# Kernel tuning notes

Measured on AMD Instinct MI355X. Metric: run time of the kernel, lower is better.

The kernel has to match this reference:

```python
import jax, jax.numpy as jnp
import numpy as np

N = 4000; T_GRU = 32; T_TREE = 16; F = 256; HS = 128; H = 3 * HS; CC = 512; E = 64000; D4 = 4 * HS


def _gru_last(x, wi, wh, bi, bh):
    # x: [N, T, F]; torch GRU gate order r, z, n. Returns last hidden [N, H].
    xp = jnp.einsum('ntf,gf->ntg', x, wi) + bi  # [N, T, 3H]
    h0 = jnp.zeros((x.shape[0], wh.shape[1]), x.dtype)
    def step(h, xt):
        gh = h @ wh.T + bh
        ir, iz, inn = jnp.split(xt, 3, axis=1)
        hr, hz, hn = jnp.split(gh, 3, axis=1)
        r = jax.nn.sigmoid(ir + hr)
        z = jax.nn.sigmoid(iz + hz)
        n = jnp.tanh(inn + r * hn)
        return (1.0 - z) * n + z * h, None
    hT, _ = jax.lax.scan(step, h0, jnp.swapaxes(xp, 0, 1))
    return hT


def _tree_root(x, ioux_w, ioux_b, iouh_w, iouh_b, fx_w, fx_b, fh_w, fh_b):
    # Chain-structured TreeLSTM (each node has one child); x: [N, T, F], leaf-to-root.
    xi = jnp.einsum('ntf,gf->ntg', x, ioux_w) + ioux_b  # [N, T, 3M]
    xf = jnp.einsum('ntf,mf->ntm', x, fx_w) + fx_b      # [N, T, M]
    M = fh_w.shape[0]
    z0 = jnp.zeros((x.shape[0], M), x.dtype)
    def step(carry, xs):
        c, h = carry
        xi_t, xf_t = xs
        iou = xi_t + h @ iouh_w.T + iouh_b
        i, o, u = jnp.split(iou, 3, axis=1)
        f = jax.nn.sigmoid(xf_t + h @ fh_w.T + fh_b)
        c = jax.nn.sigmoid(i) * jnp.tanh(u) + f * c
        h = jax.nn.sigmoid(o) * jnp.tanh(c)
        return (c, h), None
    (c, h), _ = jax.lax.scan(step, (z0, z0), (jnp.swapaxes(xi, 0, 1), jnp.swapaxes(xf, 0, 1)))
    return h


def _gcn(x, w, b, row, col):
    # PyG GCNConv: self-loops + symmetric normalization.
    n = x.shape[0]
    xw = x @ w.T
    loops = jnp.arange(n, dtype=row.dtype)
    r = jnp.concatenate([row, loops])
    c = jnp.concatenate([col, loops])
    deg = jax.ops.segment_sum(jnp.ones(r.shape, x.dtype), c, num_segments=n)
    dinv = jnp.where(deg > 0, jax.lax.rsqrt(jnp.maximum(deg, 1e-12)), 0.0)
    norm = (dinv[r] * dinv[c])[:, None]
    return jax.ops.segment_sum(xw[r] * norm, c, num_segments=n) + b


def setup_inputs() -> dict:
    key = jax.random.key(0)
    ks = jax.random.split(key, 48)
    s = 0.05
    p = lambda i, sh: jax.random.normal(ks[i], sh, jnp.float32) * s
    return {
        'feat1': p(0, (N, T_GRU, F)),
        'feat2': p(1, (N, T_TREE, F)),
        'feat3': p(2, (N, T_TREE, F)),
        'feat4': p(3, (N, CC)),
        'edge_index': jax.random.randint(ks[4], (2, E), 0, N),
        'gru_wi': p(5, (3 * H, F)), 'gru_wh': p(6, (3 * H, H)),
        'gru_bi': p(7, (3 * H,)), 'gru_bh': p(8, (3 * H,)),
        't1_ioux_w': p(9, (3 * H, F)), 't1_ioux_b': p(10, (3 * H,)),
        't1_iouh_w': p(11, (3 * H, H)), 't1_iouh_b': p(12, (3 * H,)),
        't1_fx_w': p(13, (H, F)), 't1_fx_b': p(14, (H,)),
        't1_fh_w': p(15, (H, H)), 't1_fh_b': p(16, (H,)),
        't2_ioux_w': p(17, (3 * H, F)), 't2_ioux_b': p(18, (3 * H,)),
        't2_iouh_w': p(19, (3 * H, H)), 't2_iouh_b': p(20, (3 * H,)),
        't2_fx_w': p(21, (H, F)), 't2_fx_b': p(22, (H,)),
        't2_fh_w': p(23, (H, H)), 't2_fh_b': p(24, (H,)),
        'r1_w': p(25, (HS, H)), 'r1_b': p(26, (HS,)),
        'r2_w': p(27, (HS, H)), 'r2_b': p(28, (HS,)),
        'r3_w': p(29, (HS, H)), 'r3_b': p(30, (HS,)),
        'r4_w': p(31, (HS, CC)), 'r4_b': p(32, (HS,)),
        'gcn0_w': p(33, (D4, D4)), 'gcn0_b': p(34, (D4,)),
        'gcn1_w': p(35, (D4, D4)), 'gcn1_b': p(36, (D4,)),
        'r7_w': p(37, (2, D4)), 'r7_b': p(38, (2,)),
    }


def reference(feat1, feat2, feat3, feat4, edge_index,
              gru_wi, gru_wh, gru_bi, gru_bh,
              t1_ioux_w, t1_ioux_b, t1_iouh_w, t1_iouh_b, t1_fx_w, t1_fx_b, t1_fh_w, t1_fh_b,
              t2_ioux_w, t2_ioux_b, t2_iouh_w, t2_iouh_b, t2_fx_w, t2_fx_b, t2_fh_w, t2_fh_b,
              r1_w, r1_b, r2_w, r2_b, r3_w, r3_b, r4_w, r4_b,
              gcn0_w, gcn0_b, gcn1_w, gcn1_b, r7_w, r7_b):
    v1 = _gru_last(feat1, gru_wi, gru_wh, gru_bi, gru_bh)            # [N, H]
    v2 = _tree_root(feat2, t1_ioux_w, t1_ioux_b, t1_iouh_w, t1_iouh_b, t1_fx_w, t1_fx_b, t1_fh_w, t1_fh_b)
    v3 = _tree_root(feat3, t2_ioux_w, t2_ioux_b, t2_iouh_w, t2_iouh_b, t2_fx_w, t2_fx_b, t2_fh_w, t2_fh_b)
    f1 = v1 @ r1_w.T + r1_b
    f2 = v2 @ r2_w.T + r2_b
    f3 = v3 @ r3_w.T + r3_b
    f4 = feat4 @ r4_w.T + r4_b
    m = jnp.concatenate([f1, f2, f3, f4], axis=1)                    # [N, 4*HS]
    row, col = edge_index[0], edge_index[1]
    m = jax.nn.relu(_gcn(m, gcn0_w, gcn0_b, row, col))
    m = _gcn(m, gcn1_w, gcn1_b, row, col)
    m = jax.nn.softmax(m @ r7_w.T + r7_b, axis=1)                    # [N, 2]
    return m.T                                                       # [2, N]
```

## Files before the change

### kernel.cpp

```cpp
#include <hip/hip_runtime.h>
#include <hip/hip_bf16.h>
#include <math.h>

#define NN 4000
#define TG 32
#define TT 16
#define FF 256
#define HH 384
#define GCOLS 1536
#define KCAT 640
#define EE 64000
#define D4 512

typedef __attribute__((ext_vector_type(8))) short short8;
typedef __attribute__((ext_vector_type(8))) unsigned short ushort8v;
typedef __attribute__((ext_vector_type(4))) float float4v;

static __device__ __forceinline__ float fsig(float x)  { return 1.0f / (1.0f + __expf(-x)); }
static __device__ __forceinline__ float ftanh(float x) { return 2.0f / (1.0f + __expf(-2.0f*x)) - 1.0f; }
static __device__ __forceinline__ unsigned short f2bf(float f) {
    __hip_bfloat16 h = __float2bfloat16(f); return *reinterpret_cast<unsigned short*>(&h);
}
static __device__ __forceinline__ float bf2f(unsigned short u) {
    union { unsigned int i; float f; } x; x.i = ((unsigned int)u) << 16; return x.f;
}

static __device__ __forceinline__ void async_copy16(const void* g, void* l) {
    __builtin_amdgcn_global_load_lds(
        (const __attribute__((address_space(1))) unsigned int*)g,
        (__attribute__((address_space(3))) unsigned int*)l, 16, 0, 0);
}

static __device__ __forceinline__ void xcd_swz(int& bx, int& by, int& bz) {
    const int gx = gridDim.x, gy = gridDim.y;
    const int nwg = gx * gy * gridDim.z;
    const int w = (blockIdx.z * gy + blockIdx.y) * gx + blockIdx.x;
    const int q = nwg >> 3, r = nwg & 7;
    const int xcd = w & 7, i = w >> 3;
    const int L = (xcd < r ? xcd*(q+1) : r*(q+1) + (xcd - r)*q) + i;
    bx = L % gx; int rest = L / gx;
    by = rest % gy; bz = rest / gy;
}

__global__ __launch_bounds__(256) void prep_w_kernel(
    const float* __restrict__ gwi, const float* __restrict__ gwh,
    const float* __restrict__ gbi, const float* __restrict__ gbh,
    const float* __restrict__ x1w, const float* __restrict__ x1b,
    const float* __restrict__ h1w, const float* __restrict__ h1b,
    const float* __restrict__ fx1w, const float* __restrict__ fx1b,
    const float* __restrict__ fh1w, const float* __restrict__ fh1b,
    const float* __restrict__ x2w, const float* __restrict__ x2b,
    const float* __restrict__ h2w, const float* __restrict__ h2b,
    const float* __restrict__ fx2w, const float* __restrict__ fx2b,
    const float* __restrict__ fh2w, const float* __restrict__ fh2b,
    __hip_bfloat16* __restrict__ Wx, __hip_bfloat16* __restrict__ Wh,
    float* __restrict__ bp)
{
    int z = blockIdx.z;
    int idx = blockIdx.x * 256 + threadIdx.x;
    int c = idx / KCAT, k = idx - c * KCAT;
    int bx = c >> 7, wc = (c >> 6) & 1, g = (c >> 4) & 3, rl = c & 15;
    int j = bx*32 + wc*16 + rl;
    float v = 0.0f, bv = 0.0f;
    if (z == 0) {
        if (g <= 1) {
            int row = g*HH + j;
            v = (k < FF) ? gwi[row*FF + k] : gwh[row*HH + (k-FF)];
            bv = gbi[row] + gbh[row];
        } else if (g == 2) {
            int row = 2*HH + j;
            v = (k < FF) ? gwi[row*FF + k] : 0.0f;
            bv = gbi[row];
        } else {
            int row = 2*HH + j;
            v = (k < FF) ? 0.0f : gwh[row*HH + (k-FF)];
            bv = gbh[row];
        }
    } else {
        const float* xw  = (z==1)? x1w  : x2w;   const float* xb  = (z==1)? x1b  : x2b;
        const float* hw  = (z==1)? h1w  : h2w;   const float* hb_ = (z==1)? h1b  : h2b;
        const float* fxw = (z==1)? fx1w : fx2w;  const float* fxb = (z==1)? fx1b : fx2b;
        const float* fhw = (z==1)? fh1w : fh2w;  const float* fhb = (z==1)? fh1b : fh2b;
        if (g < 3) {
            int row = g*HH + j;
            v = (k < FF) ? xw[row*FF + k] : hw[row*HH + (k-FF)];
            bv = xb[row] + hb_[row];
        } else {
            v = (k < FF) ? fxw[j*FF + k] : fhw[j*HH + (k-FF)];
            bv = fxb[j] + fhb[j];
        }
    }
    if (k < FF) Wx[(size_t)z*GCOLS*FF + (size_t)c*FF + k] = __float2bfloat16(v);
    else        Wh[(size_t)z*GCOLS*HH + (size_t)c*HH + (k-FF)] = __float2bfloat16(v);
    if (k == 0) bp[z*GCOLS + c] = bv;
}

#define C0 (TG*NN*FF/8)
#define C1 (C0 + TT*NN*FF/8)
#define C2 (C1 + TT*NN*FF/8)
#define C3 (C2 + NN*D4/8)
#define C4 (C3 + 128*HH/8)
#define C5 (C4 + 128*HH/8)
#define C6 (C5 + 128*HH/8)
#define C7 (C6 + 128*D4/8)
#define C8 (C7 + D4*D4/8)
#define C9 (C8 + D4*D4/8)

__global__ __launch_bounds__(256) void conv_all_kernel(
    const float* __restrict__ f1, const float* __restrict__ f2, const float* __restrict__ f3,
    const float* __restrict__ f4, const float* __restrict__ r1w, const float* __restrict__ r2w,
    const float* __restrict__ r3w, const float* __restrict__ r4w,
    const float* __restrict__ g0w, const float* __restrict__ g1w,
    __hip_bfloat16* __restrict__ xg, __hip_bfloat16* __restrict__ xt,
    __hip_bfloat16* __restrict__ f4b, __hip_bfloat16* __restrict__ rw123,
    __hip_bfloat16* __restrict__ r4w16, __hip_bfloat16* __restrict__ g0w16,
    __hip_bfloat16* __restrict__ g1w16)
{
    int i = blockIdx.x*256 + threadIdx.x;
    if (i >= C9) return;
    const float* s; __hip_bfloat16* d; int off;
    if      (i < C0) { s = f1;  d = xg;                      off = i; }
    else if (i < C1) { s = f2;  d = xt;                      off = i - C0; }
    else if (i < C2) { s = f3;  d = xt + (size_t)TT*NN*FF;   off = i - C1; }
    else if (i < C3) { s = f4;  d = f4b;                     off = i - C2; }
    else if (i < C4) { s = r1w; d = rw123;                   off = i - C3; }
    else if (i < C5) { s = r2w; d = rw123 + 128*HH;          off = i - C4; }
    else if (i < C6) { s = r3w; d = rw123 + 2*128*HH;        off = i - C5; }
    else if (i < C7) { s = r4w; d = r4w16;                   off = i - C6; }
    else if (i < C8) { s = g0w; d = g0w16;                   off = i - C7; }
    else             { s = g1w; d = g1w16;                   off = i - C8; }
    float4 v0 = ((const float4*)s)[off*2];
    float4 v1 = ((const float4*)s)[off*2 + 1];
    ushort8v u;
    u[0] = f2bf(v0.x); u[1] = f2bf(v0.y); u[2] = f2bf(v0.z); u[3] = f2bf(v0.w);
    u[4] = f2bf(v1.x); u[5] = f2bf(v1.y); u[6] = f2bf(v1.z); u[7] = f2bf(v1.w);
    ((ushort8v*)d)[off] = u;
}

#define BM 128
#define BN 128
#define BKK 32

__global__ __launch_bounds__(256) void gemm0_k(
    const __hip_bfloat16* __restrict__ Ab, size_t zA, int lda,
    const __hip_bfloat16* __restrict__ Wb, size_t zW, int K,
    const float* __restrict__ bias, size_t zB,
    float* __restrict__ C, size_t zC,
    __hip_bfloat16* __restrict__ C16, size_t zC16,
    int ldC, int M)
{
    const int z = blockIdx.z;
    const __hip_bfloat16* A = Ab + zA*z;
    const __hip_bfloat16* W = Wb + zW*z;

    __shared__ __align__(16) __hip_bfloat16 As[BM][BKK];
    __shared__ __align__(16) __hip_bfloat16 Bs[BN][BKK];

    const int tid  = threadIdx.x;
    const int lane = tid & 63;
    const int w    = tid >> 6;
    const int wr = w >> 1, wc = w & 1;
    const int rowBase = blockIdx.y * BM;
    const int colBase = blockIdx.x * BN;
    const int sRow = tid >> 2;
    const int sK   = (tid & 3) * 8;

    float4v acc[4][4];
    #pragma unroll
    for (int i = 0; i < 4; ++i)
        #pragma unroll
        for (int j = 0; j < 4; ++j)
            acc[i][j] = (float4v){0.f, 0.f, 0.f, 0.f};

    const int rl = lane & 15;
    const int kl = (lane >> 4) * 8;

    for (int kt = 0; kt < K; kt += BKK) {
        const int kk = kt + sK;
        #pragma unroll
        for (int i = 0; i < 2; ++i) {
            int gr = rowBase + i*64 + sRow;
            if (gr > M-1) gr = M-1;
            async_copy16(A + (size_t)gr*lda + kk, &As[i*64 + sRow][sK]);
        }
        #pragma unroll
        for (int i = 0; i < 2; ++i) {
            int r = i*64 + sRow;
            async_copy16(W + (size_t)(colBase + r)*K + kk, &Bs[r][sK]);
        }
        __syncthreads();

        short8 af[4], bfr[4];
        #pragma unroll
        for (int mi = 0; mi < 4; ++mi)
            af[mi] = *(const short8*)&As[wr*64 + mi*16 + rl][kl];
        #pragma unroll
        for (int ni = 0; ni < 4; ++ni)
            bfr[ni] = *(const short8*)&Bs[wc*64 + ni*16 + rl][kl];
        #pragma unroll
        for (int mi = 0; mi < 4; ++mi)
            #pragma unroll
            for (int ni = 0; ni < 4; ++ni)
                acc[mi][ni] = __builtin_amdgcn_mfma_f32_16x16x32_bf16(af[mi], bfr[ni], acc[mi][ni], 0, 0, 0);
        __syncthreads();
    }

    const int rq = (lane >> 4) * 4;
    float* Cz = C ? (C + zC*z) : nullptr;
    __hip_bfloat16* C16z = C16 ? (C16 + zC16*z) : nullptr;
    #pragma unroll
    for (int mi = 0; mi < 4; ++mi) {
        #pragma unroll
        for (int q = 0; q < 4; ++q) {
            int row = rowBase + wr*64 + mi*16 + rq + q;
            if (row >= M) continue;
            #pragma unroll
            for (int ni = 0; ni < 4; ++ni) {
                int col = colBase + wc*64 + ni*16 + rl;
                float v = acc[mi][ni][q];
                if (bias) v += bias[zB*z + col];
                if (Cz)   Cz[(size_t)row*ldC + col] = v;
                if (C16z) C16z[(size_t)row*ldC + col] = __float2bfloat16(v);
            }
        }
    }
}

struct StepSet {
    const __hip_bfloat16 *X, *Hin, *Wx, *Wh;
    const float *bp;
    const __hip_bfloat16 *Sin;
    __hip_bfloat16 *Sout, *Hout;
    int lda, xoff;
};

#define NT (KCAT/BKK)
#define SBM 64

template<int MODE>
__global__ __launch_bounds__(256) void step_k(StepSet S)
{
    int bxi, byi, bzi;
    xcd_swz(bxi, byi, bzi);

    const __hip_bfloat16* X  = S.X;
    const __hip_bfloat16* Hi = S.Hin;
    const __hip_bfloat16* Wx = S.Wx;
    const __hip_bfloat16* Wh = S.Wh;
    const float* bp = S.bp;
    const __hip_bfloat16* Si = S.Sin;
    __hip_bfloat16* So = S.Sout;
    __hip_bfloat16* Ho = S.Hout;
    const int lda = S.lda, xoff = S.xoff;

    __shared__ __align__(16) __hip_bfloat16 As[3][SBM][BKK];
    __shared__ __align__(16) __hip_bfloat16 Bs[3][BN][BKK];

    const int tid  = threadIdx.x;
    const int lane = tid & 63;
    const int w    = tid >> 6;
    const int wr = w >> 1, wc = w & 1;
    const int rowBase = byi * SBM;
    const int colBase = bxi * BN;

    const int sR  = tid >> 2;
    const int sC  = tid & 3;
    const int sSw = sC ^ ((sR >> 1) & 3);
    int gra = rowBase + sR; if (gra > NN-1) gra = NN-1;

    auto stage = [&](int buf, int kt) {
        if (kt < FF) {
            const int kk = kt + sSw*8;
            async_copy16(X  + (size_t)gra*lda + xoff + kk,          &As[buf][sR][sC*8]);
            async_copy16(Wx + (size_t)(colBase + sR)*FF + kk,       &Bs[buf][sR][sC*8]);
            async_copy16(Wx + (size_t)(colBase + 64 + sR)*FF + kk,  &Bs[buf][64 + sR][sC*8]);
        } else {
            const int kk = kt - FF + sSw*8;
            async_copy16(Hi + (size_t)gra*HH + kk,                  &As[buf][sR][sC*8]);
            async_copy16(Wh + (size_t)(colBase + sR)*HH + kk,       &Bs[buf][sR][sC*8]);
            async_copy16(Wh + (size_t)(colBase + 64 + sR)*HH + kk,  &Bs[buf][64 + sR][sC*8]);
        }
    };

    float4v acc[2][4];
    #pragma unroll
    for (int i = 0; i < 2; ++i)
        #pragma unroll
        for (int j = 0; j < 4; ++j)
            acc[i][j] = (float4v){0.f, 0.f, 0.f, 0.f};

    const int rl = lane & 15;
    const int dF = (lane >> 4) ^ ((rl >> 1) & 3);

    stage(0, 0);
    stage(1, BKK);

    #pragma unroll
    for (int it = 0; it < NT; ++it) {
        if (it < NT-1) asm volatile("s_waitcnt vmcnt(3)" ::: "memory");
        else           asm volatile("s_waitcnt vmcnt(0)" ::: "memory");
        __builtin_amdgcn_sched_barrier(0);
        __builtin_amdgcn_s_barrier();
        __builtin_amdgcn_sched_barrier(0);
        if (it + 2 < NT) stage((it+2)%3, (it+2)*BKK);
        __builtin_amdgcn_sched_barrier(0);

        const int cur = it % 3;
        short8 af[2], bfr[4];
        #pragma unroll
        for (int mi = 0; mi < 2; ++mi)
            af[mi] = *(const short8*)&As[cur][wr*32 + mi*16 + rl][dF*8];

        const bool xph = (it*BKK) < FF;
        if (MODE == 2) {
            #pragma unroll
            for (int ni = 0; ni < 4; ++ni)
                bfr[ni] = *(const short8*)&Bs[cur][wc*64 + ni*16 + rl][dF*8];
            asm volatile("s_waitcnt lgkmcnt(0)" ::: "memory");
            __builtin_amdgcn_sched_barrier(0);
            #pragma unroll
            for (int mi = 0; mi < 2; ++mi)
                #pragma unroll
                for (int ni = 0; ni < 4; ++ni)
                    acc[mi][ni] = __builtin_amdgcn_mfma_f32_16x16x32_bf16(af[mi], bfr[ni], acc[mi][ni], 0, 0, 0);
        } else if (xph) {
            #pragma unroll
            for (int ni = 0; ni < 3; ++ni)
                bfr[ni] = *(const short8*)&Bs[cur][wc*64 + ni*16 + rl][dF*8];
            asm volatile("s_waitcnt lgkmcnt(0)" ::: "memory");
            __builtin_amdgcn_sched_barrier(0);
            #pragma unroll
            for (int mi = 0; mi < 2; ++mi)
                #pragma unroll
                for (int ni = 0; ni < 3; ++ni)
                    acc[mi][ni] = __builtin_amdgcn_mfma_f32_16x16x32_bf16(af[mi], bfr[ni], acc[mi][ni], 0, 0, 0);
        } else {
            bfr[0] = *(const short8*)&Bs[cur][wc*64 + 0*16 + rl][dF*8];
            bfr[1] = *(const short8*)&Bs[cur][wc*64 + 1*16 + rl][dF*8];
            bfr[3] = *(const short8*)&Bs[cur][wc*64 + 3*16 + rl][dF*8];
            asm volatile("s_waitcnt lgkmcnt(0)" ::: "memory");
            __builtin_amdgcn_sched_barrier(0);
            #pragma unroll
            for (int mi = 0; mi < 2; ++mi) {
                acc[mi][0] = __builtin_amdgcn_mfma_f32_16x16x32_bf16(af[mi], bfr[0], acc[mi][0], 0, 0, 0);
                acc[mi][1] = __builtin_amdgcn_mfma_f32_16x16x32_bf16(af[mi], bfr[1], acc[mi][1], 0, 0, 0);
                acc[mi][3] = __builtin_amdgcn_mfma_f32_16x16x32_bf16(af[mi], bfr[3], acc[mi][3], 0, 0, 0);
            }
        }
    }

    const int rq = (lane >> 4) * 4;
    const int j  = (colBase >> 2) + wc*16 + rl;
    const int cb = colBase + wc*64 + rl;
    float b0 = bp[cb + 0];
    float b1 = bp[cb + 16];
    float b2 = bp[cb + 32];
    float b3 = bp[cb + 48];

    #pragma unroll
    for (int mi = 0; mi < 2; ++mi) {
        #pragma unroll
        for (int q = 0; q < 4; ++q) {
            int row = rowBase + wr*32 + mi*16 + rq + q;
            if (row >= NN) continue;
            float g0 = acc[mi][0][q] + b0;
            float g1 = acc[mi][1][q] + b1;
            float g2 = acc[mi][2][q] + b2;
            float g3 = acc[mi][3][q] + b3;
            size_t off = (size_t)row*HH + j;
            if (MODE == 1) {
                float r  = fsig(g0), zz = fsig(g1);
                float n  = ftanh(g2 + r*g3);
                float hp = __bfloat162float(Hi[off]);
                float hn = (1.0f - zz)*n + zz*hp;
                Ho[off] = __float2bfloat16(hn);
            } else {
                float cp = __bfloat162float(Si[off]);
                float cn = fsig(g0)*ftanh(g2) + fsig(g3)*cp;
                So[off] = __float2bfloat16(cn);
                float hn = fsig(g1)*ftanh(cn);
                Ho[off] = __float2bfloat16(hn);
            }
        }
    }
}

__global__ __launch_bounds__(256) void count_kernel(const int* __restrict__ col, int* __restrict__ degi)
{
    int e = blockIdx.x*256 + threadIdx.x;
    if (e < EE) atomicAdd(&degi[col[e]], 1);
}

__global__ __launch_bounds__(1024) void scan_kernel(const int* __restrict__ degi,
    int* __restrict__ start, int* __restrict__ cursor, float* __restrict__ dinv)
{
    __shared__ int s[1024];
    int t = threadIdx.x;
    int v[4]; int sum = 0;
    #pragma unroll
    for (int i = 0; i < 4; ++i) {
        int idx = t*4 + i;
        v[i] = (idx < NN) ? degi[idx] : 0;
        sum += v[i];
    }
    s[t] = sum;
    __syncthreads();
    for (int d = 1; d < 1024; d <<= 1) {
        int x = (t >= d) ? s[t-d] : 0;
        __syncthreads();
        s[t] += x;
        __syncthreads();
    }
    int base = s[t] - sum;
    int run = 0;
    #pragma unroll
    for (int i = 0; i < 4; ++i) {
        int idx = t*4 + i;
        if (idx < NN) {
            int st = base + run;
            start[idx] = st;
            cursor[idx] = st;
            dinv[idx] = rsqrtf((float)v[i] + 1.0f);
        }
        run += v[i];
    }
    if (t == 1023) start[NN] = s[1023];
}

__global__ __launch_bounds__(256) void fill_kernel(const int* __restrict__ row,
    const int* __restrict__ col, int* __restrict__ cursor, int* __restrict__ esrc)
{
    int e = blockIdx.x*256 + threadIdx.x;
    if (e < EE) {
        int c = col[e];
        int pos = atomicAdd(&cursor[c], 1);
        esrc[pos] = row[e];
    }
}

__global__ __launch_bounds__(256) void gather_kernel(const __hip_bfloat16* __restrict__ xw,
    const int* __restrict__ esrc, const int* __restrict__ start,
    const float* __restrict__ dinv, const float* __restrict__ bias,
    float* __restrict__ mout, __hip_bfloat16* __restrict__ mout16, int relu)
{
    int wv = threadIdx.x >> 6, lane = threadIdx.x & 63;
    int n = blockIdx.x*4 + wv;
    if (n >= NN) return;
    float a[8] = {0.f,0.f,0.f,0.f,0.f,0.f,0.f,0.f};
    int s0 = start[n], s1 = start[n+1];
    float dn = dinv[n];
    for (int e = s0; e < s1; ++e) {
        int r = esrc[e];
        float nrm = dinv[r]*dn;
        ushort8v v = *(const ushort8v*)(xw + (size_t)r*D4 + lane*8);
        #pragma unroll
        for (int i = 0; i < 8; ++i) a[i] += bf2f(v[i])*nrm;
    }
    ushort8v u = *(const ushort8v*)(xw + (size_t)n*D4 + lane*8);
    float dd = dn*dn;
    #pragma unroll
    for (int i = 0; i < 8; ++i) {
        float vv = a[i] + bf2f(u[i])*dd + bias[lane*8 + i];
        if (relu) vv = fmaxf(vv, 0.0f);
        if (mout)   mout[(size_t)n*D4 + lane*8 + i] = vv;
        if (mout16) mout16[(size_t)n*D4 + lane*8 + i] = __float2bfloat16(vv);
    }
}

__global__ __launch_bounds__(256) void final_kernel(const float* __restrict__ m,
    const float* __restrict__ w, const float* __restrict__ b, float* __restrict__ out)
{
    int wave = threadIdx.x >> 6;
    int lane = threadIdx.x & 63;
    int n = blockIdx.x*4 + wave;
    const float* row = m + (size_t)n*D4 + lane*8;
    float4 v0 = *(const float4*)(row);
    float4 v1 = *(const float4*)(row + 4);
    const float* w0 = w + lane*8;
    const float* w1 = w + D4 + lane*8;
    float4 u0 = *(const float4*)(w0); float4 u1 = *(const float4*)(w0 + 4);
    float4 t0 = *(const float4*)(w1); float4 t1 = *(const float4*)(w1 + 4);
    float a = v0.x*u0.x + v0.y*u0.y + v0.z*u0.z + v0.w*u0.w
            + v1.x*u1.x + v1.y*u1.y + v1.z*u1.z + v1.w*u1.w;
    float bb = v0.x*t0.x + v0.y*t0.y + v0.z*t0.z + v0.w*t0.w
             + v1.x*t1.x + v1.y*t1.y + v1.z*t1.z + v1.w*t1.w;
    #pragma unroll
    for (int s = 32; s; s >>= 1) { a += __shfl_xor(a, s); bb += __shfl_xor(bb, s); }
    if (lane == 0) {
        float l0 = a + b[0], l1 = bb + b[1];
        float mx = fmaxf(l0, l1);
        float e0 = expf(l0 - mx), e1 = expf(l1 - mx);
        float s = e0 + e1;
        out[n]      = e0 / s;
        out[NN + n] = e1 / s;
    }
}

extern "C" void kernel_launch(void* const* d_in, const int* in_sizes, int n_in,
                              void* d_out, int out_size, void* d_ws, size_t ws_size,
                              hipStream_t stream)
{
    const float* feat1 = (const float*)d_in[0];
    const float* feat2 = (const float*)d_in[1];
    const float* feat3 = (const float*)d_in[2];
    const float* feat4 = (const float*)d_in[3];
    const int*   eidx  = (const int*)d_in[4];
    const float* r1w = (const float*)d_in[25]; const float* r1b = (const float*)d_in[26];
    const float* r2w = (const float*)d_in[27]; const float* r2b = (const float*)d_in[28];
    const float* r3w = (const float*)d_in[29]; const float* r3b = (const float*)d_in[30];
    const float* r4w = (const float*)d_in[31]; const float* r4b = (const float*)d_in[32];
    const float* g0w = (const float*)d_in[33]; const float* g0b = (const float*)d_in[34];
    const float* g1w = (const float*)d_in[35]; const float* g1b = (const float*)d_in[36];
    const float* r7w = (const float*)d_in[37]; const float* r7b = (const float*)d_in[38];

    float* ws = (float*)d_ws;
    size_t o = 0;
    auto alloc = [&](size_t nfl) { float* p = ws + o; o += (nfl + 3) & ~(size_t)3; return p; };

    __hip_bfloat16* hb0 = (__hip_bfloat16*)alloc((size_t)3*NN*HH/2);
    __hip_bfloat16* cb0 = (__hip_bfloat16*)alloc((size_t)NN*HH);
    size_t zeroFloats = o;
    __hip_bfloat16* hb1 = (__hip_bfloat16*)alloc((size_t)3*NN*HH/2);
    __hip_bfloat16* cb1 = (__hip_bfloat16*)alloc((size_t)NN*HH);
    __hip_bfloat16* xg  = (__hip_bfloat16*)alloc((size_t)TG*NN*FF/2);
    __hip_bfloat16* xt  = (__hip_bfloat16*)alloc((size_t)2*TT*NN*FF/2);
    __hip_bfloat16* Wx  = (__hip_bfloat16*)alloc((size_t)3*GCOLS*FF/2);
    __hip_bfloat16* Wh  = (__hip_bfloat16*)alloc((size_t)3*GCOLS*HH/2);
    float* bp   = alloc(3*GCOLS);
    float* mbuf = alloc((size_t)NN*D4);
    __hip_bfloat16* xwb16 = (__hip_bfloat16*)alloc((size_t)NN*D4/2);
    float* dinv = alloc(NN);
    __hip_bfloat16* mbf16 = (__hip_bfloat16*)alloc((size_t)NN*D4/2);
    __hip_bfloat16* f4b   = (__hip_bfloat16*)alloc((size_t)NN*D4/2);
    __hip_bfloat16* rw123 = (__hip_bfloat16*)alloc((size_t)3*128*HH/2);
    float* rb123 = alloc(3*128);
    __hip_bfloat16* r4w16 = (__hip_bfloat16*)alloc((size_t)128*D4/2);
    __hip_bfloat16* g0w16 = (__hip_bfloat16*)alloc((size_t)D4*D4/2);
    __hip_bfloat16* g1w16 = (__hip_bfloat16*)alloc((size_t)D4*D4/2);
    int* degi   = (int*)alloc(NN);
    int* start  = (int*)alloc(NN + 4);
    int* cursor = (int*)alloc(NN);
    int* esrc   = (int*)alloc(EE);

    __hip_bfloat16* hbp[2] = {hb0, hb1};
    __hip_bfloat16* cbp[2] = {cb0, cb1};

    hipMemsetAsync(hb0, 0, zeroFloats*sizeof(float), stream);
    hipMemsetAsync(degi, 0, NN*sizeof(int), stream);

    prep_w_kernel<<<dim3(3840,1,3),256,0,stream>>>(
        (const float*)d_in[5],(const float*)d_in[6],(const float*)d_in[7],(const float*)d_in[8],
        (const float*)d_in[9],(const float*)d_in[10],(const float*)d_in[11],(const float*)d_in[12],
        (const float*)d_in[13],(const float*)d_in[14],(const float*)d_in[15],(const float*)d_in[16],
        (const float*)d_in[17],(const float*)d_in[18],(const float*)d_in[19],(const float*)d_in[20],
        (const float*)d_in[21],(const float*)d_in[22],(const float*)d_in[23],(const float*)d_in[24],
        Wx, Wh, bp);

    conv_all_kernel<<<(C9 + 255)/256,256,0,stream>>>(
        feat1, feat2, feat3, feat4, r1w, r2w, r3w, r4w, g0w, g1w,
        xg, xt, f4b, rw123, r4w16, g0w16, g1w16);
    hipMemcpyAsync(rb123,       r1b, 128*sizeof(float), hipMemcpyDeviceToDevice, stream);
    hipMemcpyAsync(rb123 + 128, r2b, 128*sizeof(float), hipMemcpyDeviceToDevice, stream);
    hipMemcpyAsync(rb123 + 256, r3b, 128*sizeof(float), hipMemcpyDeviceToDevice, stream);

    count_kernel<<<250,256,0,stream>>>(eidx + EE, degi);
    scan_kernel<<<1,1024,0,stream>>>(degi, start, cursor, dinv);
    fill_kernel<<<250,256,0,stream>>>(eidx, eidx + EE, cursor, esrc);

    for (int t = 0; t < TG; ++t) {
        int p = t & 1, q = p ^ 1;
        StepSet Gs = { xg, hbp[p], Wx, Wh, bp,
                       hbp[p], hbp[q], hbp[q], TG*FF, t*FF };
        step_k<1><<<dim3(GCOLS/BN, 63, 1),256,0,stream>>>(Gs);
    }
    for (int tr = 0; tr < 2; ++tr) {
        for (int t = 0; t < TT; ++t) {
            int p = t & 1, q = p ^ 1;
            StepSet Ts = { xt + (size_t)tr*TT*NN*FF,
                           hbp[p] + (size_t)(1+tr)*NN*HH,
                           Wx + (size_t)(1+tr)*GCOLS*FF,
                           Wh + (size_t)(1+tr)*GCOLS*HH,
                           bp + (size_t)(1+tr)*GCOLS,
                           cbp[p] + (size_t)tr*NN*HH,
                           cbp[q] + (size_t)tr*NN*HH,
                           hbp[q] + (size_t)(1+tr)*NN*HH,
                           TT*FF, t*FF };
            step_k<2><<<dim3(GCOLS/BN, 63, 1),256,0,stream>>>(Ts);
        }
    }

    gemm0_k<<<dim3(1,32,3),256,0,stream>>>(
        hbp[0], (size_t)NN*HH, HH, rw123, (size_t)128*HH, HH, rb123, 128,
        nullptr, 0, mbf16, 128, D4, NN);
    gemm0_k<<<dim3(1,32,1),256,0,stream>>>(
        f4b, 0, D4, r4w16, 0, D4, r4b, 0,
        nullptr, 0, mbf16 + 384, 0, D4, NN);

    gemm0_k<<<dim3(4,32,1),256,0,stream>>>(
        mbf16, 0, D4, g0w16, 0, D4, nullptr, 0,
        nullptr, 0, xwb16, 0, D4, NN);
    gather_kernel<<<1000,256,0,stream>>>(xwb16, esrc, start, dinv, g0b, nullptr, mbf16, 1);

    gemm0_k<<<dim3(4,32,1),256,0,stream>>>(
        mbf16, 0, D4, g1w16, 0, D4, nullptr, 0,
        nullptr, 0, xwb16, 0, D4, NN);
    gather_kernel<<<1000,256,0,stream>>>(xwb16, esrc, start, dinv, g1b, mbuf, nullptr, 0);

    final_kernel<<<1000,256,0,stream>>>(mbuf, r7w, r7b, (float*)d_out);
}
```

Before: 1.459 ms.

## Fuse fp32-to-bf16 input conversion into recurrent step kernels and merge prep launches

Step kernels now read the fp32 feature sequences directly, hold them in registers and convert to bf16 into shared memory, instead of a separate pass converting all of feat1/2/3 into bf16 buffers. The remaining small conversions, the bias copies and the degree count are merged into one prep kernel, which removes several launches and memcpys. This avoids a large read-and-write pass over the features, but each step kernel now reads twice as many bytes for its X tiles and carries extra registers plus changed wait-count bookkeeping.

```diff
diff --git a/kernel.cpp b/kernel.cpp
--- a/kernel.cpp
+++ b/kernel.cpp
@@ -95,46 +95,49 @@
     if (k == 0) bp[z*GCOLS + c] = bv;
 }
 
-#define C0 (TG*NN*FF/8)
-#define C1 (C0 + TT*NN*FF/8)
-#define C2 (C1 + TT*NN*FF/8)
-#define C3 (C2 + NN*D4/8)
-#define C4 (C3 + 128*HH/8)
-#define C5 (C4 + 128*HH/8)
-#define C6 (C5 + 128*HH/8)
-#define C7 (C6 + 128*D4/8)
-#define C8 (C7 + D4*D4/8)
-#define C9 (C8 + D4*D4/8)
-
-__global__ __launch_bounds__(256) void conv_all_kernel(
-    const float* __restrict__ f1, const float* __restrict__ f2, const float* __restrict__ f3,
+#define B0 (NN*D4/8)
+#define B1 (B0 + 128*HH/8)
+#define B2 (B1 + 128*HH/8)
+#define B3 (B2 + 128*HH/8)
+#define B4 (B3 + 128*D4/8)
+#define B5 (B4 + D4*D4/8)
+#define B6 (B5 + D4*D4/8)
+#define B7 (B6 + 384)
+#define B8 (B7 + EE)
+
+__global__ __launch_bounds__(256) void prep2_kernel(
     const float* __restrict__ f4, const float* __restrict__ r1w, const float* __restrict__ r2w,
     const float* __restrict__ r3w, const float* __restrict__ r4w,
     const float* __restrict__ g0w, const float* __restrict__ g1w,
-    __hip_bfloat16* __restrict__ xg, __hip_bfloat16* __restrict__ xt,
+    const float* __restrict__ r1b, const float* __restrict__ r2b, const float* __restrict__ r3b,
+    const int* __restrict__ col,
     __hip_bfloat16* __restrict__ f4b, __hip_bfloat16* __restrict__ rw123,
     __hip_bfloat16* __restrict__ r4w16, __hip_bfloat16* __restrict__ g0w16,
-    __hip_bfloat16* __restrict__ g1w16)
+    __hip_bfloat16* __restrict__ g1w16, float* __restrict__ rb123,
+    int* __restrict__ degi)
 {
     int i = blockIdx.x*256 + threadIdx.x;
-    if (i >= C9) return;
-    const float* s; __hip_bfloat16* d; int off;
-    if      (i < C0) { s = f1;  d = xg;                      off = i; }
-    else if (i < C1) { s = f2;  d = xt;                      off = i - C0; }
-    else if (i < C2) { s = f3;  d = xt + (size_t)TT*NN*FF;   off = i - C1; }
-    else if (i < C3) { s = f4;  d = f4b;                     off = i - C2; }
-    else if (i < C4) { s = r1w; d = rw123;                   off = i - C3; }
-    else if (i < C5) { s = r2w; d = rw123 + 128*HH;          off = i - C4; }
-    else if (i < C6) { s = r3w; d = rw123 + 2*128*HH;        off = i - C5; }
-    else if (i < C7) { s = r4w; d = r4w16;                   off = i - C6; }
-    else if (i < C8) { s = g0w; d = g0w16;                   off = i - C7; }
-    else             { s = g1w; d = g1w16;                   off = i - C8; }
-    float4 v0 = ((const float4*)s)[off*2];
-    float4 v1 = ((const float4*)s)[off*2 + 1];
-    ushort8v u;
-    u[0] = f2bf(v0.x); u[1] = f2bf(v0.y); u[2] = f2bf(v0.z); u[3] = f2bf(v0.w);
-    u[4] = f2bf(v1.x); u[5] = f2bf(v1.y); u[6] = f2bf(v1.z); u[7] = f2bf(v1.w);
-    ((ushort8v*)d)[off] = u;
+    if (i < B6) {
+        const float* s; __hip_bfloat16* d; int off;
+        if      (i < B0) { s = f4;  d = f4b;              off = i; }
+        else if (i < B1) { s = r1w; d = rw123;            off = i - B0; }
+        else if (i < B2) { s = r2w; d = rw123 + 128*HH;   off = i - B1; }
+        else if (i < B3) { s = r3w; d = rw123 + 2*128*HH; off = i - B2; }
+        else if (i < B4) { s = r4w; d = r4w16;            off = i - B3; }
+        else if (i < B5) { s = g0w; d = g0w16;            off = i - B4; }
+        else             { s = g1w; d = g1w16;            off = i - B5; }
+        float4 v0 = ((const float4*)s)[off*2];
+        float4 v1 = ((const float4*)s)[off*2 + 1];
+        ushort8v u;
+        u[0] = f2bf(v0.x); u[1] = f2bf(v0.y); u[2] = f2bf(v0.z); u[3] = f2bf(v0.w);
+        u[4] = f2bf(v1.x); u[5] = f2bf(v1.y); u[6] = f2bf(v1.z); u[7] = f2bf(v1.w);
+        ((ushort8v*)d)[off] = u;
+    } else if (i < B7) {
+        int k = i - B6;
+        rb123[k] = (k < 128) ? r1b[k] : (k < 256) ? r2b[k-128] : r3b[k-256];
+    } else if (i < B8) {
+        atomicAdd(&degi[col[i - B7]], 1);
+    }
 }
 
 #define BM 128
@@ -227,7 +230,8 @@
 }
 
 struct StepSet {
-    const __hip_bfloat16 *X, *Hin, *Wx, *Wh;
+    const float *Xf;
+    const __hip_bfloat16 *Hin, *Wx, *Wh;
     const float *bp;
     const __hip_bfloat16 *Sin;
     __hip_bfloat16 *Sout, *Hout;
@@ -235,6 +239,7 @@
 };
 
 #define NT (KCAT/BKK)
+#define XNT (FF/BKK)
 #define SBM 64
 
 template<int MODE>
@@ -243,7 +248,7 @@
     int bxi, byi, bzi;
     xcd_swz(bxi, byi, bzi);
 
-    const __hip_bfloat16* X  = S.X;
+    const float* Xf = S.Xf;
     const __hip_bfloat16* Hi = S.Hin;
     const __hip_bfloat16* Wx = S.Wx;
     const __hip_bfloat16* Wh = S.Wh;
@@ -268,18 +273,29 @@
     const int sSw = sC ^ ((sR >> 1) & 3);
     int gra = rowBase + sR; if (gra > NN-1) gra = NN-1;
 
-    auto stage = [&](int buf, int kt) {
-        if (kt < FF) {
-            const int kk = kt + sSw*8;
-            async_copy16(X  + (size_t)gra*lda + xoff + kk,          &As[buf][sR][sC*8]);
-            async_copy16(Wx + (size_t)(colBase + sR)*FF + kk,       &Bs[buf][sR][sC*8]);
-            async_copy16(Wx + (size_t)(colBase + 64 + sR)*FF + kk,  &Bs[buf][64 + sR][sC*8]);
-        } else {
-            const int kk = kt - FF + sSw*8;
-            async_copy16(Hi + (size_t)gra*HH + kk,                  &As[buf][sR][sC*8]);
-            async_copy16(Wh + (size_t)(colBase + sR)*HH + kk,       &Bs[buf][sR][sC*8]);
-            async_copy16(Wh + (size_t)(colBase + 64 + sR)*HH + kk,  &Bs[buf][64 + sR][sC*8]);
-        }
+    float4 xr0a, xr0b, xr1a, xr1b;
+
+    auto stageX = [&](int set, int buf, int kt) {
+        const int kk = kt + sSw*8;
+        const float* src = Xf + (size_t)gra*lda + xoff + kk;
+        if (set == 0) { xr0a = *(const float4*)src; xr0b = *(const float4*)(src + 4); }
+        else          { xr1a = *(const float4*)src; xr1b = *(const float4*)(src + 4); }
+        async_copy16(Wx + (size_t)(colBase + sR)*FF + kk,       &Bs[buf][sR][sC*8]);
+        async_copy16(Wx + (size_t)(colBase + 64 + sR)*FF + kk,  &Bs[buf][64 + sR][sC*8]);
+    };
+    auto commitX = [&](int set, int buf) {
+        float4 a = set ? xr1a : xr0a;
+        float4 b = set ? xr1b : xr0b;
+        ushort8v u;
+        u[0] = f2bf(a.x); u[1] = f2bf(a.y); u[2] = f2bf(a.z); u[3] = f2bf(a.w);
+        u[4] = f2bf(b.x); u[5] = f2bf(b.y); u[6] = f2bf(b.z); u[7] = f2bf(b.w);
+        *(ushort8v*)&As[buf][sR][sC*8] = u;
+    };
+    auto stageH = [&](int buf, int kt) {
+        const int kk = kt - FF + sSw*8;
+        async_copy16(Hi + (size_t)gra*HH + kk,                  &As[buf][sR][sC*8]);
+        async_copy16(Wh + (size_t)(colBase + sR)*HH + kk,       &Bs[buf][sR][sC*8]);
+        async_copy16(Wh + (size_t)(colBase + 64 + sR)*HH + kk,  &Bs[buf][64 + sR][sC*8]);
     };
 
     float4v acc[2][4];
@@ -292,17 +308,26 @@
     const int rl = lane & 15;
     const int dF = (lane >> 4) ^ ((rl >> 1) & 3);
 
-    stage(0, 0);
-    stage(1, BKK);
+    stageX(0, 0, 0);
+    stageX(1, 1, BKK);
 
     #pragma unroll
     for (int it = 0; it < NT; ++it) {
-        if (it < NT-1) asm volatile("s_waitcnt vmcnt(3)" ::: "memory");
-        else           asm volatile("s_waitcnt vmcnt(0)" ::: "memory");
+        if (it + 1 < XNT)      asm volatile("s_waitcnt vmcnt(4)" ::: "memory");
+        else if (it < NT - 1)  asm volatile("s_waitcnt vmcnt(3)" ::: "memory");
+        else                   asm volatile("s_waitcnt vmcnt(0)" ::: "memory");
         __builtin_amdgcn_sched_barrier(0);
+        if (it < XNT) {
+            commitX(it & 1, it % 3);
+            asm volatile("s_waitcnt lgkmcnt(0)" ::: "memory");
+            __builtin_amdgcn_sched_barrier(0);
+        }
         __builtin_amdgcn_s_barrier();
         __builtin_amdgcn_sched_barrier(0);
-        if (it + 2 < NT) stage((it+2)%3, (it+2)*BKK);
+        if (it + 2 < NT) {
+            if (it + 2 < XNT) stageX((it+2) & 1, (it+2) % 3, (it+2)*BKK);
+            else              stageH((it+2) % 3, (it+2)*BKK);
+        }
         __builtin_amdgcn_sched_barrier(0);
 
         const int cur = it % 3;
@@ -311,7 +336,7 @@
         for (int mi = 0; mi < 2; ++mi)
             af[mi] = *(const short8*)&As[cur][wr*32 + mi*16 + rl][dF*8];
 
-        const bool xph = (it*BKK) < FF;
+        const bool xph = it < XNT;
         if (MODE == 2) {
             #pragma unroll
             for (int ni = 0; ni < 4; ++ni)
@@ -385,12 +410,6 @@
     }
 }
 
-__global__ __launch_bounds__(256) void count_kernel(const int* __restrict__ col, int* __restrict__ degi)
-{
-    int e = blockIdx.x*256 + threadIdx.x;
-    if (e < EE) atomicAdd(&degi[col[e]], 1);
-}
-
 __global__ __launch_bounds__(1024) void scan_kernel(const int* __restrict__ degi,
     int* __restrict__ start, int* __restrict__ cursor, float* __restrict__ dinv)
 {
@@ -522,8 +541,6 @@
     size_t zeroFloats = o;
     __hip_bfloat16* hb1 = (__hip_bfloat16*)alloc((size_t)3*NN*HH/2);
     __hip_bfloat16* cb1 = (__hip_bfloat16*)alloc((size_t)NN*HH);
-    __hip_bfloat16* xg  = (__hip_bfloat16*)alloc((size_t)TG*NN*FF/2);
-    __hip_bfloat16* xt  = (__hip_bfloat16*)alloc((size_t)2*TT*NN*FF/2);
     __hip_bfloat16* Wx  = (__hip_bfloat16*)alloc((size_t)3*GCOLS*FF/2);
     __hip_bfloat16* Wh  = (__hip_bfloat16*)alloc((size_t)3*GCOLS*HH/2);
     float* bp   = alloc(3*GCOLS);
@@ -556,27 +573,24 @@
         (const float*)d_in[21],(const float*)d_in[22],(const float*)d_in[23],(const float*)d_in[24],
         Wx, Wh, bp);
 
-    conv_all_kernel<<<(C9 + 255)/256,256,0,stream>>>(
-        feat1, feat2, feat3, feat4, r1w, r2w, r3w, r4w, g0w, g1w,
-        xg, xt, f4b, rw123, r4w16, g0w16, g1w16);
-    hipMemcpyAsync(rb123,       r1b, 128*sizeof(float), hipMemcpyDeviceToDevice, stream);
-    hipMemcpyAsync(rb123 + 128, r2b, 128*sizeof(float), hipMemcpyDeviceToDevice, stream);
-    hipMemcpyAsync(rb123 + 256, r3b, 128*sizeof(float), hipMemcpyDeviceToDevice, stream);
-
-    count_kernel<<<250,256,0,stream>>>(eidx + EE, degi);
+    prep2_kernel<<<(B8 + 255)/256,256,0,stream>>>(
+        feat4, r1w, r2w, r3w, r4w, g0w, g1w, r1b, r2b, r3b, eidx + EE,
+        f4b, rw123, r4w16, g0w16, g1w16, rb123, degi);
+
     scan_kernel<<<1,1024,0,stream>>>(degi, start, cursor, dinv);
     fill_kernel<<<250,256,0,stream>>>(eidx, eidx + EE, cursor, esrc);
 
     for (int t = 0; t < TG; ++t) {
         int p = t & 1, q = p ^ 1;
-        StepSet Gs = { xg, hbp[p], Wx, Wh, bp,
+        StepSet Gs = { feat1, hbp[p], Wx, Wh, bp,
                        hbp[p], hbp[q], hbp[q], TG*FF, t*FF };
         step_k<1><<<dim3(GCOLS/BN, 63, 1),256,0,stream>>>(Gs);
     }
     for (int tr = 0; tr < 2; ++tr) {
+        const float* ft = tr ? feat3 : feat2;
         for (int t = 0; t < TT; ++t) {
             int p = t & 1, q = p ^ 1;
-            StepSet Ts = { xt + (size_t)tr*TT*NN*FF,
+            StepSet Ts = { ft,
                            hbp[p] + (size_t)(1+tr)*NN*HH,
                            Wx + (size_t)(1+tr)*GCOLS*FF,
                            Wh + (size_t)(1+tr)*GCOLS*HH,
```

Result: slower. 1.504 ms (+3.1%).
